# Kernel optimization log

Measured on AMD Instinct MI355X. Metric: run time of the kernel, lower is better.

## Reference

```python
import jax, jax.numpy as jnp
import numpy as np

MAX_DIST = 35.0
GRID_RES = 1.0
BOX = int(np.ceil(2 * MAX_DIST / GRID_RES + 1))  # 71


def setup_inputs() -> dict:
    key = jax.random.key(0)
    k1, k2 = jax.random.split(key)
    B, N, F = 8, 16384, 32
    # spread ~N(0, 20): most points inside [-35, 35] box, some outside (mask path)
    coords = jax.random.normal(k1, (B, N, 3), dtype=jnp.float32) * 20.0
    features = jax.random.normal(k2, (B, N, F), dtype=jnp.float32)
    return {"coords": coords, "features": features}


def reference(coords, features):
    B, N, _ = coords.shape
    F = features.shape[2]
    # quantize coords to integer grid cells
    gc = jnp.round((coords + MAX_DIST) / GRID_RES).astype(jnp.int32)  # [B,N,3]
    in_box = jnp.all((gc >= 0) & (gc < BOX), axis=2)                  # [B,N]
    # jit-friendly equivalent of boolean_mask+scatter_nd: zero out-of-box
    # updates and clamp their indices (adding zero is a no-op).
    gc_c = jnp.clip(gc, 0, BOX - 1)
    upd = jnp.where(in_box[..., None], features, 0.0)                 # [B,N,F]
    grid = jnp.zeros((B, BOX, BOX, BOX, F), dtype=features.dtype)
    # FAITHFUL to original: batch index column is tf.zeros -> every point
    # scatters (with duplicate-index summation) into batch slice 0.
    grid = grid.at[0, gc_c[..., 0], gc_c[..., 1], gc_c[..., 2]].add(upd)
    return grid
```

## Files before the change

### kernel.cpp

```cpp
#include <hip/hip_runtime.h>

#define BOX 71
#define NF 32
#define MAX_DIST_F 35.0f


__global__ __launch_bounds__(256) void MakeGrid_scatter_kernel(
    const float* __restrict__ coords,
    const float* __restrict__ features,
    float* __restrict__ grid,
    int total_points)
{
    int t = blockIdx.x * blockDim.x + threadIdx.x;
    int p = t >> 5;
    int f = t & 31;
    if (p >= total_points) return;

    float cx = coords[p * 3 + 0];
    float cy = coords[p * 3 + 1];
    float cz = coords[p * 3 + 2];

    int gx = (int)rintf(cx + MAX_DIST_F);
    int gy = (int)rintf(cy + MAX_DIST_F);
    int gz = (int)rintf(cz + MAX_DIST_F);

    bool in_box = (gx >= 0) & (gx < BOX) &
                  (gy >= 0) & (gy < BOX) &
                  (gz >= 0) & (gz < BOX);
    if (!in_box) return;

    float v = features[(size_t)p * NF + f];
    size_t idx = (((size_t)gx * BOX + gy) * BOX + gz) * NF + f;
#if defined(__AMDGCN__)
    unsafeAtomicAdd(grid + idx, v);
#else
    atomicAdd(grid + idx, v);
#endif
}

extern "C" void kernel_launch(void* const* d_in, const int* in_sizes, int n_in,
                              void* d_out, int out_size, void* d_ws, size_t ws_size,
                              hipStream_t stream) {
    const float* coords   = (const float*)d_in[0];
    const float* features = (const float*)d_in[1];
    float* out = (float*)d_out;

    hipMemsetAsync(out, 0, (size_t)out_size, stream);

    int total_points = in_sizes[0] / 3;
    int total_threads = total_points * NF;
    int blocks = (total_threads + 255) / 256;
    MakeGrid_scatter_kernel<<<blocks, 256, 0, stream>>>(coords, features, out, total_points);
}
```

Measured before the change: 328.1 us.

## Replace atomic scatter with counting-sort binning and per-cell ordered gather

Replaces the float atomic scatter with a counting sort: per-cell counts, offsets allocated through an atomic cursor, a fill pass that records point indices per cell, and a gather kernel in which each cell sums its points' features in ascending index order and writes slice 0 directly. The memset now clears only batch slices 1-7, because the gather overwrites slice 0. This removes contention on float atomics to hot cells and makes the summation order deterministic, at the cost of four kernel launches, extra workspace traffic and a per-cell O(n^2) sort that can be expensive for dense cells near the grid centre. If the workspace is too small it falls back to the original kernel.

```diff
diff --git a/kernel.cpp b/kernel.cpp
--- a/kernel.cpp
+++ b/kernel.cpp
@@ -3,38 +3,98 @@
 #define BOX 71
 #define NF 32
 #define MAX_DIST_F 35.0f
+#define NCELLS (BOX * BOX * BOX)
+#define SLICE_FLOATS (NCELLS * NF)
+#define SLICE_BYTES  ((size_t)SLICE_FLOATS * 4)
 
 
-__global__ __launch_bounds__(256) void MakeGrid_scatter_kernel(
-    const float* __restrict__ coords,
-    const float* __restrict__ features,
-    float* __restrict__ grid,
-    int total_points)
-{
-    int t = blockIdx.x * blockDim.x + threadIdx.x;
-    int p = t >> 5;
-    int f = t & 31;
-    if (p >= total_points) return;
-
+__device__ __forceinline__ bool point_cell(const float* __restrict__ coords,
+                                           int p, int& cell) {
     float cx = coords[p * 3 + 0];
     float cy = coords[p * 3 + 1];
     float cz = coords[p * 3 + 2];
-
     int gx = (int)rintf(cx + MAX_DIST_F);
     int gy = (int)rintf(cy + MAX_DIST_F);
     int gz = (int)rintf(cz + MAX_DIST_F);
-
     bool in_box = (gx >= 0) & (gx < BOX) &
                   (gy >= 0) & (gy < BOX) &
                   (gz >= 0) & (gz < BOX);
-    if (!in_box) return;
+    cell = (gx * BOX + gy) * BOX + gz;
+    return in_box;
+}
 
+__global__ __launch_bounds__(256) void count_kernel(
+    const float* __restrict__ coords, unsigned* __restrict__ cnt, int total_points)
+{
+    int p = blockIdx.x * 256 + threadIdx.x;
+    if (p >= total_points) return;
+    int c; if (!point_cell(coords, p, c)) return;
+    atomicAdd(&cnt[c], 1u);
+}
+
+__global__ __launch_bounds__(256) void offsets_kernel(
+    const unsigned* __restrict__ cnt, unsigned* __restrict__ offs,
+    unsigned* __restrict__ cursor)
+{
+    int c = blockIdx.x * 256 + threadIdx.x;
+    if (c >= NCELLS) return;
+    unsigned n = cnt[c];
+    if (n) offs[c] = atomicAdd(cursor, n);
+}
+
+__global__ __launch_bounds__(256) void fill_kernel(
+    const float* __restrict__ coords, unsigned* __restrict__ fillc,
+    const unsigned* __restrict__ offs, unsigned* __restrict__ bins,
+    int total_points)
+{
+    int p = blockIdx.x * 256 + threadIdx.x;
+    if (p >= total_points) return;
+    int c; if (!point_cell(coords, p, c)) return;
+    unsigned slot = atomicAdd(&fillc[c], 1u);
+    bins[offs[c] + slot] = (unsigned)p;
+}
+
+__global__ __launch_bounds__(256) void gather_kernel(
+    const float* __restrict__ features, const unsigned* __restrict__ cnt,
+    const unsigned* __restrict__ offs, const unsigned* __restrict__ bins,
+    float* __restrict__ grid)
+{
+    int t = blockIdx.x * 256 + threadIdx.x;
+    int c = t >> 5;
+    int f = t & 31;
+    if (c >= NCELLS) return;
+
+    int n = (int)cnt[c];
+    float acc = 0.f;
+    if (n) {
+        unsigned off = offs[c];
+        int prev = -1;
+        for (int j = 0; j < n; ++j) {
+            int m = 0x7fffffff;
+            for (int i = 0; i < n; ++i) {
+                int q = (int)bins[off + i];
+                if (q > prev && q < m) m = q;
+            }
+            acc += features[(size_t)m * NF + f];
+            prev = m;
+        }
+    }
+    grid[(size_t)c * NF + f] = acc;
+}
+
+__global__ __launch_bounds__(256) void MakeGrid_scatter_kernel(
+    const float* __restrict__ coords, const float* __restrict__ features,
+    float* __restrict__ grid, int total_points)
+{
+    int t = blockIdx.x * blockDim.x + threadIdx.x;
+    int p = t >> 5, f = t & 31;
+    if (p >= total_points) return;
+    int c; if (!point_cell(coords, p, c)) return;
     float v = features[(size_t)p * NF + f];
-    size_t idx = (((size_t)gx * BOX + gy) * BOX + gz) * NF + f;
 #if defined(__AMDGCN__)
-    unsafeAtomicAdd(grid + idx, v);
+    unsafeAtomicAdd(grid + (size_t)c * NF + f, v);
 #else
-    atomicAdd(grid + idx, v);
+    atomicAdd(grid + (size_t)c * NF + f, v);
 #endif
 }
 
@@ -45,10 +105,32 @@
     const float* features = (const float*)d_in[1];
     float* out = (float*)d_out;
 
-    hipMemsetAsync(out, 0, (size_t)out_size, stream);
+    int total_points = in_sizes[0] / 3;
 
-    int total_points = in_sizes[0] / 3;
-    int total_threads = total_points * NF;
-    int blocks = (total_threads + 255) / 256;
-    MakeGrid_scatter_kernel<<<blocks, 256, 0, stream>>>(coords, features, out, total_points);
+    size_t ws_need = ((size_t)3 * NCELLS + 1 + (size_t)total_points) * 4;
+    if (ws_size < ws_need) {
+        hipMemsetAsync(out, 0, (size_t)out_size, stream);
+        int blocks = (total_points * NF + 255) / 256;
+        MakeGrid_scatter_kernel<<<blocks, 256, 0, stream>>>(coords, features, out, total_points);
+        return;
+    }
+
+    unsigned* wsb    = (unsigned*)d_ws;
+    unsigned* cnt    = wsb;
+    unsigned* fillc  = wsb + NCELLS;
+    unsigned* cursor = wsb + 2 * (size_t)NCELLS;
+    unsigned* offs   = wsb + 2 * (size_t)NCELLS + 1;
+    unsigned* bins   = wsb + 3 * (size_t)NCELLS + 1;
+
+    hipMemsetAsync(out + SLICE_FLOATS, 0, 7 * SLICE_BYTES, stream);
+    hipMemsetAsync(wsb, 0, (2 * (size_t)NCELLS + 1) * 4, stream);
+
+    int pblocks = (total_points + 255) / 256;
+    int cblocks = (NCELLS + 255) / 256;
+    int gblocks = (NCELLS * NF + 255) / 256;
+
+    count_kernel  <<<pblocks, 256, 0, stream>>>(coords, cnt, total_points);
+    offsets_kernel<<<cblocks, 256, 0, stream>>>(cnt, offs, cursor);
+    fill_kernel   <<<pblocks, 256, 0, stream>>>(coords, fillc, offs, bins, total_points);
+    gather_kernel <<<gblocks, 256, 0, stream>>>(features, cnt, offs, bins, out);
 }
```

New measurement: 485.5 us. +48.0%, slower.
